# Optimization experiments

Measured on AMD Instinct MI355X. Metric: run time of the kernel, lower is better.

Reference implementation:

```python
import jax, jax.numpy as jnp
import numpy as np

N = 30000   # vertices
E = 4000    # hyperedges
NNZ = 960000
D = 256
ALPHA = 0.1
BETA = 0.8


def setup_inputs() -> dict:
    key = jax.random.key(0)
    k1, k2, k3, k4, k5, k6 = jax.random.split(key, 6)
    X = jax.random.normal(k1, (N, D), dtype=jnp.float32)
    X0 = jax.random.normal(k2, (N, D), dtype=jnp.float32)
    H = jax.random.uniform(k3, (N, E), dtype=jnp.float32)
    vertex = jax.random.randint(k4, (NNZ,), 0, N, dtype=jnp.int64)
    edges = jax.random.randint(k5, (NNZ,), 0, E, dtype=jnp.int64)
    # Linear(in_features=256, out_features=256, bias=False) weight, torch layout [out, in]
    W = jax.random.normal(k6, (D, D), dtype=jnp.float32) * (1.0 / np.sqrt(D))
    return {"X": X, "X0": X0, "H": H, "W": W, "vertex": vertex, "edges": edges}


def reference(X, X0, H, W, vertex, edges):
    # degree scalings from dense incidence matrix
    degV = jnp.sum(H, axis=1) ** -0.5            # [N]
    degV = jnp.where(jnp.isinf(degV), 1.0, degV)[:, None]
    degE = (jnp.sum(H, axis=0) ** -0.5)[:, None]  # [E,1]

    Xve = X[vertex]                               # [nnz, d] gather
    # scatter-mean to edges
    sums = jax.ops.segment_sum(Xve, edges, num_segments=E)            # [E, d]
    cnt = jax.ops.segment_sum(jnp.ones((Xve.shape[0],), X.dtype), edges, num_segments=E)
    Xe = sums / jnp.maximum(cnt, 1.0)[:, None]
    Xe = Xe * degE

    Xev = Xe[edges]                               # [nnz, d] gather
    Xv = jax.ops.segment_sum(Xev, vertex, num_segments=X.shape[0])    # [N, d]
    Xv = Xv * degV

    Xi = (1.0 - ALPHA) * Xv + ALPHA * X0
    out = (1.0 - BETA) * Xi + BETA * (Xi @ W.T)
    return out
```

## Files before the change

### kernel.cpp

```cpp
#include <hip/hip_runtime.h>

#define D 256
#define ALPHA 0.1f
#define BETA 0.8f
#define CAPE 384
#define CAPV 96

typedef float v4f __attribute__((ext_vector_type(4)));

__device__ __forceinline__ void add4(float4& a, const float4& b) {
    a.x += b.x; a.y += b.y; a.z += b.z; a.w += b.w;
}

__device__ __forceinline__ unsigned short f2bf(float f) {
    unsigned int u = __float_as_uint(f);
    u += 0x7FFFu + ((u >> 16) & 1u);
    return (unsigned short)(u >> 16);
}
__device__ __forceinline__ float bf2f(unsigned short h) {
    return __uint_as_float((unsigned int)h << 16);
}
__device__ __forceinline__ void addbf4(float4& a, const ushort4& t) {
    a.x += bf2f(t.x); a.y += bf2f(t.y); a.z += bf2f(t.z); a.w += bf2f(t.w);
}

__global__ __launch_bounds__(256) void k_init(const float* __restrict__ W,
                                              float* __restrict__ Wt,
                                              float* __restrict__ colsum,
                                              int* __restrict__ cnt_e,
                                              int* __restrict__ cnt_v,
                                              const float* __restrict__ X,
                                              unsigned short* __restrict__ Xb,
                                              int n, int e, int total4) {
    int idx = blockIdx.x * 256 + threadIdx.x;
    if (idx < total4) {
        float4 x = reinterpret_cast<const float4*>(X)[idx];
        ushort4 b;
        b.x = f2bf(x.x); b.y = f2bf(x.y); b.z = f2bf(x.z); b.w = f2bf(x.w);
        reinterpret_cast<ushort4*>(Xb)[idx] = b;
    }
    if (idx < D * D) {
        int o = idx >> 8, i = idx & 255;
        Wt[i * D + o] = BETA * W[o * D + i] + ((i == o) ? (1.0f - BETA) : 0.0f);
    }
    if (idx < e) { colsum[idx] = 0.f; cnt_e[idx] = 0; }
    if (idx < n) cnt_v[idx] = 0;
}

__global__ __launch_bounds__(256) void k_build(const float* __restrict__ H,
                                               float* __restrict__ rowsum,
                                               float* __restrict__ colsum,
                                               const int* __restrict__ vertex,
                                               const int* __restrict__ edges,
                                               int* __restrict__ cnt_e,
                                               int* __restrict__ cnt_v,
                                               int* __restrict__ list_e,
                                               int* __restrict__ list_v,
                                               int n, int e, int nnz) {
    const int tid = threadIdx.x;
    const int b   = blockIdx.x;

    if ((b & 1) == 0) {
        const int rid  = b >> 1;
        const int wave = tid >> 6, lane = tid & 63;
        const int ec4  = e >> 2;
        __shared__ float4 sl[4][1000];

        float4 cp[16];
        #pragma unroll
        for (int k = 0; k < 16; ++k) cp[k] = make_float4(0.f, 0.f, 0.f, 0.f);

        const int rbase = rid * 32 + wave * 8;
        for (int i = 0; i < 8; ++i) {
            int row = rbase + i;
            float rs = 0.f;
            if (row < n) {
                const v4f* Hr = reinterpret_cast<const v4f*>(H + (size_t)row * e);
                float4 v[16];
                #pragma unroll
                for (int k = 0; k < 16; ++k) {
                    int s = lane + 64 * k;
                    if (s < ec4) {
                        v4f t = __builtin_nontemporal_load(Hr + s);
                        v[k] = make_float4(t.x, t.y, t.z, t.w);
                    } else {
                        v[k] = make_float4(0.f, 0.f, 0.f, 0.f);
                    }
                }
                #pragma unroll
                for (int k = 0; k < 16; ++k) {
                    rs += (v[k].x + v[k].y) + (v[k].z + v[k].w);
                    add4(cp[k], v[k]);
                }
            }
            #pragma unroll
            for (int s = 32; s > 0; s >>= 1) rs += __shfl_down(rs, s, 64);
            if (lane == 0 && row < n) rowsum[row] = rs;
        }

        #pragma unroll
        for (int k = 0; k < 16; ++k) {
            int s = lane + 64 * k;
            if (s < ec4) sl[wave][s] = cp[k];
        }
        __syncthreads();

        for (int c4 = tid; c4 < ec4; c4 += 256) {
            float4 s = sl[0][c4];
            add4(s, sl[1][c4]); add4(s, sl[2][c4]); add4(s, sl[3][c4]);
            atomicAdd(&colsum[4 * c4 + 0], s.x);
            atomicAdd(&colsum[4 * c4 + 1], s.y);
            atomicAdd(&colsum[4 * c4 + 2], s.z);
            atomicAdd(&colsum[4 * c4 + 3], s.w);
        }
    } else {
        const int fid = b >> 1;
        int base4 = ((fid * 256) + tid) * 4;
        if (base4 + 3 < nnz) {
            int4 ee = reinterpret_cast<const int4*>(edges)[base4 >> 2];
            int4 vv = reinterpret_cast<const int4*>(vertex)[base4 >> 2];
            int p0 = atomicAdd(&cnt_e[ee.x], 1);
            int p1 = atomicAdd(&cnt_e[ee.y], 1);
            int p2 = atomicAdd(&cnt_e[ee.z], 1);
            int p3 = atomicAdd(&cnt_e[ee.w], 1);
            int q0 = atomicAdd(&cnt_v[vv.x], 1);
            int q1 = atomicAdd(&cnt_v[vv.y], 1);
            int q2 = atomicAdd(&cnt_v[vv.z], 1);
            int q3 = atomicAdd(&cnt_v[vv.w], 1);
            if (p0 < CAPE) list_e[(size_t)ee.x * CAPE + p0] = vv.x;
            if (p1 < CAPE) list_e[(size_t)ee.y * CAPE + p1] = vv.y;
            if (p2 < CAPE) list_e[(size_t)ee.z * CAPE + p2] = vv.z;
            if (p3 < CAPE) list_e[(size_t)ee.w * CAPE + p3] = vv.w;
            if (q0 < CAPV) list_v[(size_t)vv.x * CAPV + q0] = ee.x;
            if (q1 < CAPV) list_v[(size_t)vv.y * CAPV + q1] = ee.y;
            if (q2 < CAPV) list_v[(size_t)vv.z * CAPV + q2] = ee.z;
            if (q3 < CAPV) list_v[(size_t)vv.w * CAPV + q3] = ee.w;
        } else {
            for (int i = base4; i < nnz; ++i) {
                int ee = edges[i], v = vertex[i];
                int p = atomicAdd(&cnt_e[ee], 1);
                if (p < CAPE) list_e[(size_t)ee * CAPE + p] = v;
                int q = atomicAdd(&cnt_v[v], 1);
                if (q < CAPV) list_v[(size_t)v * CAPV + q] = ee;
            }
        }
    }
}

__global__ __launch_bounds__(256) void k_edge_agg(const unsigned short* __restrict__ Xb,
                                                  const int* __restrict__ list_e,
                                                  const int* __restrict__ cnt_e,
                                                  const float* __restrict__ colsum,
                                                  unsigned short* __restrict__ Xeb, int e) {
    const int eid  = blockIdx.x * 4 + (threadIdx.x >> 6);
    const int lane = threadIdx.x & 63;
    if (eid >= e) return;
    const int cnt  = cnt_e[eid];
    const int m    = cnt < CAPE ? cnt : CAPE;
    const int j0   = eid * CAPE;

    float4 a[8];
    #pragma unroll
    for (int k = 0; k < 8; ++k) a[k] = make_float4(0.f, 0.f, 0.f, 0.f);

    int j = 0;
    for (; j + 7 < m; j += 8) {
        #pragma unroll
        for (int k = 0; k < 8; ++k) {
            int v = list_e[j0 + j + k];
            ushort4 t = reinterpret_cast<const ushort4*>(Xb + (size_t)v * D)[lane];
            addbf4(a[k], t);
        }
    }
    for (; j < m; ++j) {
        int v = list_e[j0 + j];
        ushort4 t = reinterpret_cast<const ushort4*>(Xb + (size_t)v * D)[lane];
        addbf4(a[0], t);
    }
    #pragma unroll
    for (int k = 1; k < 8; ++k) add4(a[0], a[k]);

    float scale = rsqrtf(colsum[eid]) / (float)(cnt > 0 ? cnt : 1);
    ushort4 o;
    o.x = f2bf(a[0].x * scale); o.y = f2bf(a[0].y * scale);
    o.z = f2bf(a[0].z * scale); o.w = f2bf(a[0].w * scale);
    reinterpret_cast<ushort4*>(Xeb + (size_t)eid * D)[lane] = o;
}

__global__ __launch_bounds__(256) void k_vertex_agg(const unsigned short* __restrict__ Xeb,
                                                    const int* __restrict__ list_v,
                                                    const int* __restrict__ cnt_v,
                                                    const float* __restrict__ rowsum,
                                                    const float* __restrict__ X0,
                                                    float* __restrict__ Xi, int n) {
    const int v    = blockIdx.x * 4 + (threadIdx.x >> 6);
    const int lane = threadIdx.x & 63;
    if (v >= n) return;
    const int cnt  = cnt_v[v];
    const int m    = cnt < CAPV ? cnt : CAPV;
    const int j0   = v * CAPV;

    float4 a[4];
    #pragma unroll
    for (int k = 0; k < 4; ++k) a[k] = make_float4(0.f, 0.f, 0.f, 0.f);

    int j = 0;
    for (; j + 3 < m; j += 4) {
        #pragma unroll
        for (int k = 0; k < 4; ++k) {
            int e = list_v[j0 + j + k];
            ushort4 t = reinterpret_cast<const ushort4*>(Xeb + (size_t)e * D)[lane];
            addbf4(a[k], t);
        }
    }
    for (; j < m; ++j) {
        int e = list_v[j0 + j];
        ushort4 t = reinterpret_cast<const ushort4*>(Xeb + (size_t)e * D)[lane];
        addbf4(a[0], t);
    }
    add4(a[0], a[1]); add4(a[2], a[3]); add4(a[0], a[2]);

    float rs = rowsum[v];
    float degV = (rs > 0.f) ? rsqrtf(rs) : 1.0f;
    float scale = (1.0f - ALPHA) * degV;
    float4 x0 = reinterpret_cast<const float4*>(X0 + (size_t)v * D)[lane];
    float4 o;
    o.x = scale * a[0].x + ALPHA * x0.x;
    o.y = scale * a[0].y + ALPHA * x0.y;
    o.z = scale * a[0].z + ALPHA * x0.z;
    o.w = scale * a[0].w + ALPHA * x0.w;
    reinterpret_cast<float4*>(Xi + (size_t)v * D)[lane] = o;
}

__global__ __launch_bounds__(256) void k_gemm(const float* __restrict__ A,
                                              const float* __restrict__ B,
                                              float* __restrict__ C, int n) {
    const int BM = 128, BN = 128, BK = 16;
    __shared__ float As[BK][BM + 4];
    __shared__ float Bs[BK][BN];
    const int row0 = blockIdx.x * BM;
    const int col0 = blockIdx.y * BN;
    const int tid = threadIdx.x;
    const int tx = tid & 15, ty = tid >> 4;

    float c[8][8];
    #pragma unroll
    for (int i = 0; i < 8; ++i)
        #pragma unroll
        for (int j = 0; j < 8; ++j) c[i][j] = 0.f;

    for (int kk = 0; kk < D; kk += BK) {
        #pragma unroll
        for (int h = 0; h < 2; ++h) {
            int idx = tid + h * 256;
            int r = idx >> 2, cq = idx & 3;
            int row = row0 + r;
            float4 a = (row < n)
                ? reinterpret_cast<const float4*>(A + (size_t)row * D + kk)[cq]
                : make_float4(0.f, 0.f, 0.f, 0.f);
            As[cq * 4 + 0][r] = a.x;
            As[cq * 4 + 1][r] = a.y;
            As[cq * 4 + 2][r] = a.z;
            As[cq * 4 + 3][r] = a.w;
        }
        #pragma unroll
        for (int h = 0; h < 2; ++h) {
            int idx = tid + h * 256;
            int k = idx >> 5, c4 = idx & 31;
            float4 b = reinterpret_cast<const float4*>(B + (size_t)(kk + k) * D + col0)[c4];
            reinterpret_cast<float4*>(&Bs[k][c4 * 4])[0] = b;
        }
        __syncthreads();
        #pragma unroll
        for (int k = 0; k < BK; ++k) {
            float4 a0 = *reinterpret_cast<const float4*>(&As[k][ty * 8]);
            float4 a1 = *reinterpret_cast<const float4*>(&As[k][ty * 8 + 4]);
            float4 b0 = *reinterpret_cast<const float4*>(&Bs[k][tx * 8]);
            float4 b1 = *reinterpret_cast<const float4*>(&Bs[k][tx * 8 + 4]);
            float av[8] = {a0.x, a0.y, a0.z, a0.w, a1.x, a1.y, a1.z, a1.w};
            float bv[8] = {b0.x, b0.y, b0.z, b0.w, b1.x, b1.y, b1.z, b1.w};
            #pragma unroll
            for (int i = 0; i < 8; ++i)
                #pragma unroll
                for (int j = 0; j < 8; ++j)
                    c[i][j] = fmaf(av[i], bv[j], c[i][j]);
        }
        __syncthreads();
    }
    #pragma unroll
    for (int i = 0; i < 8; ++i) {
        int row = row0 + ty * 8 + i;
        if (row < n) {
            float4 o0 = make_float4(c[i][0], c[i][1], c[i][2], c[i][3]);
            float4 o1 = make_float4(c[i][4], c[i][5], c[i][6], c[i][7]);
            float4* p = reinterpret_cast<float4*>(C + (size_t)row * D + col0 + tx * 8);
            p[0] = o0; p[1] = o1;
        }
    }
}

extern "C" void kernel_launch(void* const* d_in, const int* in_sizes, int n_in,
                              void* d_out, int out_size, void* d_ws, size_t ws_size,
                              hipStream_t stream) {
    const float* X      = (const float*)d_in[0];
    const float* X0     = (const float*)d_in[1];
    const float* H      = (const float*)d_in[2];
    const float* W      = (const float*)d_in[3];
    const int*   vertex = (const int*)d_in[4];
    const int*   edges  = (const int*)d_in[5];
    float* out = (float*)d_out;

    const int n   = in_sizes[0] / D;
    const int e   = in_sizes[2] / n;
    const int nnz = in_sizes[4];

    char* base = (char*)d_ws;
    size_t off = 0;
    auto carve = [&](size_t bytes) {
        size_t o = off;
        off += (bytes + 255) & ~(size_t)255;
        return o;
    };
    float*          Xi     = (float*)(base + carve((size_t)n * D * 4));
    unsigned short* Xb     = (unsigned short*)(base + carve((size_t)n * D * 2));
    unsigned short* Xeb    = (unsigned short*)(base + carve((size_t)e * D * 2));
    float*          Wt     = (float*)(base + carve((size_t)D * D * 4));
    float*          rowsum = (float*)(base + carve((size_t)n * 4));
    float*          colsum = (float*)(base + carve((size_t)e * 4));
    int*            cnt_e  = (int*)(base + carve((size_t)e * 4));
    int*            cnt_v  = (int*)(base + carve((size_t)n * 4));
    int*            list_e = (int*)(base + carve((size_t)e * CAPE * 4));
    int*            list_v = (int*)(base + carve((size_t)n * CAPV * 4));
    (void)ws_size; (void)n_in; (void)out_size;

    const int nRowBlk  = (n + 31) / 32;
    const int nFillBlk = (nnz / 4 + 255) / 256;
    const int total4   = n * D / 4;
    const int nInitBlk = (total4 + 255) / 256;

    k_init<<<dim3(nInitBlk), dim3(256), 0, stream>>>(W, Wt, colsum, cnt_e, cnt_v,
                                                     X, Xb, n, e, total4);
    k_build<<<dim3(nRowBlk + nFillBlk), dim3(256), 0, stream>>>(
        H, rowsum, colsum, vertex, edges, cnt_e, cnt_v, list_e, list_v, n, e, nnz);
    k_edge_agg<<<dim3((e + 3) / 4), dim3(256), 0, stream>>>(Xb, list_e, cnt_e, colsum, Xeb, e);
    k_vertex_agg<<<dim3((n + 3) / 4), dim3(256), 0, stream>>>(Xeb, list_v, cnt_v, rowsum, X0, Xi, n);
    k_gemm<<<dim3((n + 127) / 128, D / 128), dim3(256), 0, stream>>>(Xi, Wt, out, n);
}
```

Before: 366.5 us.

## Replace fp32 SIMT GEMM with bf16 MFMA GEMM and store Xi as bf16

The vertex aggregation now writes Xi in bf16, and the folded weight matrix is stored in bf16 in its original [out,in] layout. A new GEMM kernel has each wave compute a 16x256 output strip with mfma_f32_16x16x32_bf16, loading A and B fragments straight from global memory with no LDS staging. This removes the fp32 FMA-bound GEMM and halves the Xi traffic, at the cost of bf16 rounding of Xi and W. The output stores are scattered 4-byte writes, and n must be a multiple of 16.

```diff
diff --git a/kernel.cpp b/kernel.cpp
--- a/kernel.cpp
+++ b/kernel.cpp
@@ -7,6 +7,8 @@
 #define CAPV 96
 
 typedef float v4f __attribute__((ext_vector_type(4)));
+typedef float f32x4 __attribute__((ext_vector_type(4)));
+typedef short bf16x8 __attribute__((ext_vector_type(8)));
 
 __device__ __forceinline__ void add4(float4& a, const float4& b) {
     a.x += b.x; a.y += b.y; a.z += b.z; a.w += b.w;
@@ -25,7 +27,7 @@
 }
 
 __global__ __launch_bounds__(256) void k_init(const float* __restrict__ W,
-                                              float* __restrict__ Wt,
+                                              unsigned short* __restrict__ Wtb,
                                               float* __restrict__ colsum,
                                               int* __restrict__ cnt_e,
                                               int* __restrict__ cnt_v,
@@ -41,7 +43,7 @@
     }
     if (idx < D * D) {
         int o = idx >> 8, i = idx & 255;
-        Wt[i * D + o] = BETA * W[o * D + i] + ((i == o) ? (1.0f - BETA) : 0.0f);
+        Wtb[idx] = f2bf(BETA * W[idx] + ((i == o) ? (1.0f - BETA) : 0.0f));
     }
     if (idx < e) { colsum[idx] = 0.f; cnt_e[idx] = 0; }
     if (idx < n) cnt_v[idx] = 0;
@@ -192,7 +194,7 @@
                                                     const int* __restrict__ cnt_v,
                                                     const float* __restrict__ rowsum,
                                                     const float* __restrict__ X0,
-                                                    float* __restrict__ Xi, int n) {
+                                                    unsigned short* __restrict__ Xib, int n) {
     const int v    = blockIdx.x * 4 + (threadIdx.x >> 6);
     const int lane = threadIdx.x & 63;
     if (v >= n) return;
@@ -224,77 +226,46 @@
     float degV = (rs > 0.f) ? rsqrtf(rs) : 1.0f;
     float scale = (1.0f - ALPHA) * degV;
     float4 x0 = reinterpret_cast<const float4*>(X0 + (size_t)v * D)[lane];
-    float4 o;
-    o.x = scale * a[0].x + ALPHA * x0.x;
-    o.y = scale * a[0].y + ALPHA * x0.y;
-    o.z = scale * a[0].z + ALPHA * x0.z;
-    o.w = scale * a[0].w + ALPHA * x0.w;
-    reinterpret_cast<float4*>(Xi + (size_t)v * D)[lane] = o;
-}
-
-__global__ __launch_bounds__(256) void k_gemm(const float* __restrict__ A,
-                                              const float* __restrict__ B,
-                                              float* __restrict__ C, int n) {
-    const int BM = 128, BN = 128, BK = 16;
-    __shared__ float As[BK][BM + 4];
-    __shared__ float Bs[BK][BN];
-    const int row0 = blockIdx.x * BM;
-    const int col0 = blockIdx.y * BN;
-    const int tid = threadIdx.x;
-    const int tx = tid & 15, ty = tid >> 4;
-
-    float c[8][8];
-    #pragma unroll
-    for (int i = 0; i < 8; ++i)
-        #pragma unroll
-        for (int j = 0; j < 8; ++j) c[i][j] = 0.f;
-
-    for (int kk = 0; kk < D; kk += BK) {
-        #pragma unroll
-        for (int h = 0; h < 2; ++h) {
-            int idx = tid + h * 256;
-            int r = idx >> 2, cq = idx & 3;
-            int row = row0 + r;
-            float4 a = (row < n)
-                ? reinterpret_cast<const float4*>(A + (size_t)row * D + kk)[cq]
-                : make_float4(0.f, 0.f, 0.f, 0.f);
-            As[cq * 4 + 0][r] = a.x;
-            As[cq * 4 + 1][r] = a.y;
-            As[cq * 4 + 2][r] = a.z;
-            As[cq * 4 + 3][r] = a.w;
-        }
-        #pragma unroll
-        for (int h = 0; h < 2; ++h) {
-            int idx = tid + h * 256;
-            int k = idx >> 5, c4 = idx & 31;
-            float4 b = reinterpret_cast<const float4*>(B + (size_t)(kk + k) * D + col0)[c4];
-            reinterpret_cast<float4*>(&Bs[k][c4 * 4])[0] = b;
-        }
-        __syncthreads();
-        #pragma unroll
-        for (int k = 0; k < BK; ++k) {
-            float4 a0 = *reinterpret_cast<const float4*>(&As[k][ty * 8]);
-            float4 a1 = *reinterpret_cast<const float4*>(&As[k][ty * 8 + 4]);
-            float4 b0 = *reinterpret_cast<const float4*>(&Bs[k][tx * 8]);
-            float4 b1 = *reinterpret_cast<const float4*>(&Bs[k][tx * 8 + 4]);
-            float av[8] = {a0.x, a0.y, a0.z, a0.w, a1.x, a1.y, a1.z, a1.w};
-            float bv[8] = {b0.x, b0.y, b0.z, b0.w, b1.x, b1.y, b1.z, b1.w};
-            #pragma unroll
-            for (int i = 0; i < 8; ++i)
-                #pragma unroll
-                for (int j = 0; j < 8; ++j)
-                    c[i][j] = fmaf(av[i], bv[j], c[i][j]);
-        }
-        __syncthreads();
-    }
-    #pragma unroll
-    for (int i = 0; i < 8; ++i) {
-        int row = row0 + ty * 8 + i;
-        if (row < n) {
-            float4 o0 = make_float4(c[i][0], c[i][1], c[i][2], c[i][3]);
-            float4 o1 = make_float4(c[i][4], c[i][5], c[i][6], c[i][7]);
-            float4* p = reinterpret_cast<float4*>(C + (size_t)row * D + col0 + tx * 8);
-            p[0] = o0; p[1] = o1;
+    ushort4 o;
+    o.x = f2bf(scale * a[0].x + ALPHA * x0.x);
+    o.y = f2bf(scale * a[0].y + ALPHA * x0.y);
+    o.z = f2bf(scale * a[0].z + ALPHA * x0.z);
+    o.w = f2bf(scale * a[0].w + ALPHA * x0.w);
+    reinterpret_cast<ushort4*>(Xib + (size_t)v * D)[lane] = o;
+}
+
+__global__ __launch_bounds__(256) void k_gemm_mfma(const unsigned short* __restrict__ A,
+                                                   const unsigned short* __restrict__ B,
+                                                   float* __restrict__ C, int n) {
+    const int wave = threadIdx.x >> 6;
+    const int lane = threadIdx.x & 63;
+    const int m0 = (blockIdx.x * 4 + wave) * 16;
+    if (m0 >= n) return;
+    const int arow = lane & 15;
+    const int kgrp = lane >> 4;
+
+    f32x4 acc[16];
+    #pragma unroll
+    for (int c = 0; c < 16; ++c) acc[c] = (f32x4){0.f, 0.f, 0.f, 0.f};
+
+    const unsigned short* aptr = A + (size_t)(m0 + arow) * D + kgrp * 8;
+    const unsigned short* bptr = B + (size_t)arow * D + kgrp * 8;
+
+    for (int kk = 0; kk < D; kk += 32) {
+        bf16x8 afrag = *reinterpret_cast<const bf16x8*>(aptr + kk);
+        #pragma unroll
+        for (int c = 0; c < 16; ++c) {
+            bf16x8 bfrag = *reinterpret_cast<const bf16x8*>(bptr + (size_t)c * 16 * D + kk);
+            acc[c] = __builtin_amdgcn_mfma_f32_16x16x32_bf16(afrag, bfrag, acc[c], 0, 0, 0);
+        }
+    }
+
+    #pragma unroll
+    for (int c = 0; c < 16; ++c) {
+        #pragma unroll
+        for (int r = 0; r < 4; ++r) {
+            int row = m0 + kgrp * 4 + r;
+            C[(size_t)row * D + c * 16 + arow] = acc[c][r];
         }
     }
 }
@@ -321,10 +292,10 @@
         off += (bytes + 255) & ~(size_t)255;
         return o;
     };
-    float*          Xi     = (float*)(base + carve((size_t)n * D * 4));
+    unsigned short* Xib    = (unsigned short*)(base + carve((size_t)n * D * 2));
     unsigned short* Xb     = (unsigned short*)(base + carve((size_t)n * D * 2));
     unsigned short* Xeb    = (unsigned short*)(base + carve((size_t)e * D * 2));
-    float*          Wt     = (float*)(base + carve((size_t)D * D * 4));
+    unsigned short* Wtb    = (unsigned short*)(base + carve((size_t)D * D * 2));
     float*          rowsum = (float*)(base + carve((size_t)n * 4));
     float*          colsum = (float*)(base + carve((size_t)e * 4));
     int*            cnt_e  = (int*)(base + carve((size_t)e * 4));
@@ -338,11 +309,11 @@
     const int total4   = n * D / 4;
     const int nInitBlk = (total4 + 255) / 256;
 
-    k_init<<<dim3(nInitBlk), dim3(256), 0, stream>>>(W, Wt, colsum, cnt_e, cnt_v,
+    k_init<<<dim3(nInitBlk), dim3(256), 0, stream>>>(W, Wtb, colsum, cnt_e, cnt_v,
                                                      X, Xb, n, e, total4);
     k_build<<<dim3(nRowBlk + nFillBlk), dim3(256), 0, stream>>>(
         H, rowsum, colsum, vertex, edges, cnt_e, cnt_v, list_e, list_v, n, e, nnz);
     k_edge_agg<<<dim3((e + 3) / 4), dim3(256), 0, stream>>>(Xb, list_e, cnt_e, colsum, Xeb, e);
-    k_vertex_agg<<<dim3((n + 3) / 4), dim3(256), 0, stream>>>(Xeb, list_v, cnt_v, rowsum, X0, Xi, n);
-    k_gemm<<<dim3((n + 127) / 128, D / 128), dim3(256), 0, stream>>>(Xi, Wt, out, n);
-}
+    k_vertex_agg<<<dim3((n + 3) / 4), dim3(256), 0, stream>>>(Xeb, list_v, cnt_v, rowsum, X0, Xib, n);
+    k_gemm_mfma<<<dim3((n / 16 + 3) / 4), dim3(256), 0, stream>>>(Xib, Wtb, out, n);
+}
```

New measurement: 403.2 us. 10.0% more time.
